# Performance work log

Measured on AMD Instinct MI355X. Metric: run time of the kernel, lower is better.

The kernel has to match this reference:

```python
import jax, jax.numpy as jnp
import numpy as np

N = 100000
E = 1600000
C_IN = 32
HEADS = 4
C = 32          # per-head out channels
L = 3           # num layers = num_hidden_layers + 1
NEG_SLOPE = 0.2


def setup_inputs() -> dict:
    key = jax.random.key(0)
    ks = jax.random.split(key, 8)
    x = jax.random.normal(ks[0], (N, C_IN), dtype=jnp.float32)
    edge_index = jax.random.randint(ks[1], (2, E), 0, N, dtype=jnp.int64)
    edge_attr = jax.random.normal(ks[2], (E, 8), dtype=jnp.float32)  # unused by GATConv (edge_dim=None)
    scale = 1.0 / np.sqrt(C_IN)
    Ws = jax.random.normal(ks[3], (L, C_IN, HEADS * C), dtype=jnp.float32) * scale
    att_src = jax.random.normal(ks[4], (L, HEADS, C), dtype=jnp.float32) * scale
    att_dst = jax.random.normal(ks[5], (L, HEADS, C), dtype=jnp.float32) * scale
    bias = jnp.zeros((L, C), dtype=jnp.float32)
    return {"x": x, "edge_index": edge_index, "edge_attr": edge_attr,
            "Ws": Ws, "att_src": att_src, "att_dst": att_dst, "bias": bias}


def _gat_layer(x, src, dst, W, a_src, a_dst, b):
    # x: [N, C_in]; src/dst: [E'] (self-loops included); W: [C_in, H*C]
    h = (x @ W).reshape(N, HEADS, C)                      # [N, H, C]
    alpha_src = jnp.sum(h * a_src, axis=-1)               # [N, H]
    alpha_dst = jnp.sum(h * a_dst, axis=-1)               # [N, H]
    e = alpha_src[src] + alpha_dst[dst]                   # [E', H]
    e = jnp.where(e > 0, e, NEG_SLOPE * e)                # leaky_relu
    # segment softmax over incoming edges of each dst node
    m = jax.ops.segment_max(e, dst, num_segments=N)       # [N, H]
    ex = jnp.exp(e - m[dst])
    s = jax.ops.segment_sum(ex, dst, num_segments=N)      # [N, H]
    alpha = ex / (s[dst] + 1e-16)                         # [E', H]
    msg = h[src] * alpha[:, :, None]                      # [E', H, C]
    out = jax.ops.segment_sum(msg, dst, num_segments=N)   # [N, H, C]
    return out.mean(axis=1) + b                           # concat=False -> mean over heads, + bias


def reference(x, edge_index, edge_attr, Ws, att_src, att_dst, bias):
    # add self loops once (GATConv add_self_loops=True)
    loops = jnp.arange(N, dtype=edge_index.dtype)
    src = jnp.concatenate([edge_index[0], loops])
    dst = jnp.concatenate([edge_index[1], loops])
    # edge_attr unused: GATConv built without edge_dim.
    # Dropout layers are identity in eval mode.
    for l in range(L):
        x = _gat_layer(x, src, dst, Ws[l], att_src[l], att_dst[l], bias[l])
        x = jax.nn.elu(x)
    return x
```

## Files before the change

kernel.cpp:

```cpp
#include <hip/hip_runtime.h>
#include <hip/hip_bf16.h>
#include <hip/hip_fp16.h>
#include <cstdint>


__global__ void k_scan1(const int* __restrict__ deg, int n, int* __restrict__ bsums) {
    __shared__ int s[256];
    int t = threadIdx.x;
    int i = blockIdx.x * 256 + t;
    int v = (i < n) ? deg[i] : 0;
    s[t] = v; __syncthreads();
    for (int off = 128; off > 0; off >>= 1) {
        if (t < off) s[t] += s[t + off];
        __syncthreads();
    }
    if (t == 0) bsums[blockIdx.x] = s[0];
}

__global__ void k_scan2(const int* __restrict__ bsums, int nb, int* __restrict__ boffs) {
    __shared__ int s[512];
    int t = threadIdx.x;
    int v = (t < nb) ? bsums[t] : 0;
    s[t] = v; __syncthreads();
    for (int off = 1; off < 512; off <<= 1) {
        int nv = (t >= off) ? s[t - off] : 0;
        __syncthreads();
        s[t] += nv;
        __syncthreads();
    }
    if (t < nb) boffs[t] = s[t] - v;
}

__global__ void k_scan3(const int* __restrict__ deg, int n, const int* __restrict__ boffs,
                        int* __restrict__ rowst) {
    __shared__ int s[256];
    int t = threadIdx.x;
    int i = blockIdx.x * 256 + t;
    int v = (i < n) ? deg[i] : 0;
    s[t] = v; __syncthreads();
    for (int off = 1; off < 256; off <<= 1) {
        int nv = (t >= off) ? s[t - off] : 0;
        __syncthreads();
        s[t] += nv;
        __syncthreads();
    }
    int incl = s[t] + boffs[blockIdx.x];
    if (i < n) {
        rowst[i] = incl - v;
        if (i == n - 1) rowst[n] = incl;
    }
}

__global__ void k_scatter(const int* __restrict__ src, const int* __restrict__ dst,
                          const int* __restrict__ rank, const int* __restrict__ rowst,
                          int E, int* __restrict__ col) {
    int t = blockIdx.x * blockDim.x + threadIdx.x;
    int base = t * 16;
    if (base + 16 <= E) {
        int4 d[4], s[4], r[4];
#pragma unroll
        for (int k = 0; k < 4; ++k) {
            d[k] = *reinterpret_cast<const int4*>(dst + base + k * 4);
            s[k] = *reinterpret_cast<const int4*>(src + base + k * 4);
            r[k] = *reinterpret_cast<const int4*>(rank + base + k * 4);
        }
        const int* dd = reinterpret_cast<const int*>(d);
        const int* ss = reinterpret_cast<const int*>(s);
        const int* rr = reinterpret_cast<const int*>(r);
        int p[16];
#pragma unroll
        for (int k = 0; k < 16; ++k) p[k] = rowst[dd[k]] + rr[k];
#pragma unroll
        for (int k = 0; k < 16; ++k) col[p[k]] = ss[k];
    } else {
        for (int i = base; i < E; ++i) col[rowst[dst[i]] + rank[i]] = src[i];
    }
}


__device__ __forceinline__ float lane_bcast(float v, int k) {
    return __int_as_float(__builtin_amdgcn_readlane(__float_as_int(v), k));
}

__global__ void __launch_bounds__(256)
k_gemm_alpha(const float* __restrict__ x, const float* __restrict__ W,
             const float* __restrict__ a_src, const float* __restrict__ a_dst,
             __half* __restrict__ h16, float* __restrict__ alpha_src,
             float* __restrict__ alpha_dst, int n,
             const int* __restrict__ dstv, int E, int* __restrict__ deg,
             int* __restrict__ rank, int gemmBlocks) {
    if ((int)blockIdx.x >= gemmBlocks) {
        int b = blockIdx.x - gemmBlocks;
        int base = (b * 256 + threadIdx.x) * 32;
        if (base + 32 <= E) {
            int4 d[8];
#pragma unroll
            for (int k = 0; k < 8; ++k)
                d[k] = *reinterpret_cast<const int4*>(dstv + base + k * 4);
            const int* dd = reinterpret_cast<const int*>(d);
            int r[32];
#pragma unroll
            for (int k = 0; k < 32; ++k) r[k] = atomicAdd(&deg[dd[k]], 1);
#pragma unroll
            for (int k = 0; k < 8; ++k)
                *reinterpret_cast<int4*>(rank + base + k * 4) =
                    *reinterpret_cast<const int4*>(r + k * 4);
        } else {
            for (int i = base; i < E; ++i) rank[i] = atomicAdd(&deg[dstv[i]], 1);
        }
        return;
    }
    int lane = threadIdx.x & 63;
    int wave = threadIdx.x >> 6;
    int j2 = lane * 2;
    int nbase = blockIdx.x * 64 + wave * 16;

    float2 wr[32];
#pragma unroll
    for (int k = 0; k < 32; ++k)
        wr[k] = *reinterpret_cast<const float2*>(W + k * 128 + j2);
    float2 as2 = *reinterpret_cast<const float2*>(a_src + j2);
    float2 ad2 = *reinterpret_cast<const float2*>(a_dst + j2);

    float xr[16];
#pragma unroll
    for (int m = 0; m < 16; ++m) {
        int node = nbase + m;
        xr[m] = (node < n) ? x[(size_t)node * 32 + (lane & 31)] : 0.f;
    }

#pragma unroll
    for (int m = 0; m < 16; ++m) {
        int node = nbase + m;
        if (node >= n) continue;
        float acc0 = 0.f, acc1 = 0.f;
#pragma unroll
        for (int k = 0; k < 32; ++k) {
            float xv = lane_bcast(xr[m], k);
            acc0 += xv * wr[k].x;
            acc1 += xv * wr[k].y;
        }
        *reinterpret_cast<__half2*>(h16 + (size_t)node * 128 + j2) =
            __floats2half2_rn(acc0, acc1);
        float ps = acc0 * as2.x + acc1 * as2.y;
        float pd = acc0 * ad2.x + acc1 * ad2.y;
#pragma unroll
        for (int mm = 1; mm < 16; mm <<= 1) {
            ps += __shfl_xor(ps, mm, 64);
            pd += __shfl_xor(pd, mm, 64);
        }
        if ((lane & 15) == 0) {
            int head = lane >> 4;
            alpha_src[node * 4 + head] = ps;
            alpha_dst[node * 4 + head] = pd;
        }
    }
}

__device__ __forceinline__ float lrelu_exp(float e) {
    e = e > 0.f ? e : 0.2f * e;
    return __expf(e);
}

__device__ __forceinline__ float4 h16_to_f4(uint2 v) {
    float2 fa = __half22float2(*reinterpret_cast<__half2*>(&v.x));
    float2 fb = __half22float2(*reinterpret_cast<__half2*>(&v.y));
    return make_float4(fa.x, fa.y, fb.x, fb.y);
}

__global__ void k_agg(const __half* __restrict__ h16, const float* __restrict__ asrc,
                      const float* __restrict__ adst, const int* __restrict__ rowst,
                      const int* __restrict__ col, const float* __restrict__ bias,
                      float* __restrict__ out, int n) {
    int wid = (int)((blockIdx.x * (size_t)blockDim.x + threadIdx.x) >> 6);
    if (wid >= n) return;
    int lane = threadIdx.x & 63;
    int half = lane >> 5;
    int q = lane & 31;
    int head = q >> 3;
    float ad = adst[wid * 4 + head];

    float4 acc = make_float4(0.f, 0.f, 0.f, 0.f);
    float s = 0.f;
    if (half == 0) {
        float w = lrelu_exp(asrc[wid * 4 + head] + ad);
        uint2 v = *reinterpret_cast<const uint2*>(h16 + (size_t)wid * 128 + q * 4);
        float4 hv = h16_to_f4(v);
        s = w;
        acc.x = w * hv.x; acc.y = w * hv.y; acc.z = w * hv.z; acc.w = w * hv.w;
    }

    int beg = rowst[wid], end = rowst[wid + 1];
    int i = beg;
    for (; i + 8 <= end; i += 8) {
        int base = i + half * 4;
        int s0 = col[base], s1 = col[base + 1], s2 = col[base + 2], s3 = col[base + 3];
        float x0 = asrc[s0 * 4 + head];
        float x1 = asrc[s1 * 4 + head];
        float x2 = asrc[s2 * 4 + head];
        float x3 = asrc[s3 * 4 + head];
        uint2 v0 = *reinterpret_cast<const uint2*>(h16 + (size_t)s0 * 128 + q * 4);
        uint2 v1 = *reinterpret_cast<const uint2*>(h16 + (size_t)s1 * 128 + q * 4);
        uint2 v2 = *reinterpret_cast<const uint2*>(h16 + (size_t)s2 * 128 + q * 4);
        uint2 v3 = *reinterpret_cast<const uint2*>(h16 + (size_t)s3 * 128 + q * 4);
        float w0 = lrelu_exp(x0 + ad);
        float w1 = lrelu_exp(x1 + ad);
        float w2 = lrelu_exp(x2 + ad);
        float w3 = lrelu_exp(x3 + ad);
        float4 h0 = h16_to_f4(v0), h1 = h16_to_f4(v1), h2 = h16_to_f4(v2), h3 = h16_to_f4(v3);
        s += w0 + w1 + w2 + w3;
        acc.x += w0 * h0.x + w1 * h1.x + w2 * h2.x + w3 * h3.x;
        acc.y += w0 * h0.y + w1 * h1.y + w2 * h2.y + w3 * h3.y;
        acc.z += w0 * h0.z + w1 * h1.z + w2 * h2.z + w3 * h3.z;
        acc.w += w0 * h0.w + w1 * h1.w + w2 * h2.w + w3 * h3.w;
    }
    for (; i + 2 <= end; i += 2) {
        int sidx = col[i + half];
        float w = lrelu_exp(asrc[sidx * 4 + head] + ad);
        float4 hv = h16_to_f4(*reinterpret_cast<const uint2*>(h16 + (size_t)sidx * 128 + q * 4));
        s += w;
        acc.x += w * hv.x; acc.y += w * hv.y; acc.z += w * hv.z; acc.w += w * hv.w;
    }
    if (i < end && half == 0) {
        int sidx = col[i];
        float w = lrelu_exp(asrc[sidx * 4 + head] + ad);
        float4 hv = h16_to_f4(*reinterpret_cast<const uint2*>(h16 + (size_t)sidx * 128 + q * 4));
        s += w;
        acc.x += w * hv.x; acc.y += w * hv.y; acc.z += w * hv.z; acc.w += w * hv.w;
    }

    s += __shfl_xor(s, 32, 64);
    acc.x += __shfl_xor(acc.x, 32, 64);
    acc.y += __shfl_xor(acc.y, 32, 64);
    acc.z += __shfl_xor(acc.z, 32, 64);
    acc.w += __shfl_xor(acc.w, 32, 64);
    float inv = 1.f / s;
    acc.x *= inv; acc.y *= inv; acc.z *= inv; acc.w *= inv;
    acc.x += __shfl_xor(acc.x, 8, 64);  acc.x += __shfl_xor(acc.x, 16, 64);
    acc.y += __shfl_xor(acc.y, 8, 64);  acc.y += __shfl_xor(acc.y, 16, 64);
    acc.z += __shfl_xor(acc.z, 8, 64);  acc.z += __shfl_xor(acc.z, 16, 64);
    acc.w += __shfl_xor(acc.w, 8, 64);  acc.w += __shfl_xor(acc.w, 16, 64);
    if (lane < 8) {
        float4 b4 = *reinterpret_cast<const float4*>(&bias[lane * 4]);
        float o0 = acc.x * 0.25f + b4.x;
        float o1 = acc.y * 0.25f + b4.y;
        float o2 = acc.z * 0.25f + b4.z;
        float o3 = acc.w * 0.25f + b4.w;
        o0 = o0 > 0.f ? o0 : (__expf(o0) - 1.f);
        o1 = o1 > 0.f ? o1 : (__expf(o1) - 1.f);
        o2 = o2 > 0.f ? o2 : (__expf(o2) - 1.f);
        o3 = o3 > 0.f ? o3 : (__expf(o3) - 1.f);
        *reinterpret_cast<float4*>(&out[(size_t)wid * 32 + lane * 4]) =
            make_float4(o0, o1, o2, o3);
    }
}


extern "C" void kernel_launch(void* const* d_in, const int* in_sizes, int n_in,
                              void* d_out, int out_size, void* d_ws, size_t ws_size,
                              hipStream_t stream) {
    const float* x       = (const float*)d_in[0];
    const int*   ei      = (const int*)d_in[1];
    const float* Ws      = (const float*)d_in[3];
    const float* att_src = (const float*)d_in[4];
    const float* att_dst = (const float*)d_in[5];
    const float* bias    = (const float*)d_in[6];

    int N = in_sizes[0] / 32;
    int E = in_sizes[1] / 2;
    const int* srcv = ei;
    const int* dstv = ei + E;

    float* fws   = (float*)d_ws;
    __half* h16  = (__half*)fws;
    float* asrc  = (float*)(h16 + (size_t)N * 128);
    float* adst  = asrc + (size_t)N * 4;
    float* xbuf  = adst + (size_t)N * 4;
    int*   deg    = (int*)(xbuf + (size_t)N * 32);
    int*   rowst  = deg + N;
    int*   bsums  = rowst + N + 1;
    int*   boffs  = bsums + 512;
    int*   col    = boffs + 512;
    int*   rank   = col + E;

    int nb256 = (N + 255) / 256;
    int gemmBlocks = (N + 63) / 64;
    int histBlocks = (E + 32 * 256 - 1) / (32 * 256);
    int scatBlocks = (E + 16 * 256 - 1) / (16 * 256);

    hipMemsetAsync(deg, 0, (size_t)N * sizeof(int), stream);

    for (int l = 0; l < 3; ++l) {
        const float* xin = (l == 0) ? x : xbuf;
        float* xout = (l == 2) ? (float*)d_out : xbuf;
        int extra = (l == 0) ? histBlocks : 0;
        k_gemm_alpha<<<gemmBlocks + extra, 256, 0, stream>>>(
            xin, Ws + (size_t)l * 32 * 128, att_src + l * 128, att_dst + l * 128,
            h16, asrc, adst, N, dstv, E, deg, rank, gemmBlocks);
        if (l == 0) {
            k_scan1<<<nb256, 256, 0, stream>>>(deg, N, bsums);
            k_scan2<<<1, 512, 0, stream>>>(bsums, nb256, boffs);
            k_scan3<<<nb256, 256, 0, stream>>>(deg, N, boffs, rowst);
            k_scatter<<<scatBlocks, 256, 0, stream>>>(srcv, dstv, rank, rowst, E, col);
        }
        k_agg<<<(N + 3) / 4, 256, 0, stream>>>(
            h16, asrc, adst, rowst, col, bias + l * 32, xout, N);
    }
}
```

Before: 437.7 us.

## Split aggregation wavefront into four 16-lane edge groups with 16-byte loads

The aggregation kernel now splits each wavefront into four 16-lane groups. Each lane loads 8 fp16 features (uint4) per neighbor instead of 4, so four edges are gathered concurrently instead of two. This is meant to raise memory-level parallelism and use wider gathers for short adjacency lists. In exchange it needs more accumulator registers and more cross-lane shuffle reductions, and lanes go idle when a node's degree is not a multiple of four.

```diff
diff --git a/kernel.cpp b/kernel.cpp
--- a/kernel.cpp
+++ b/kernel.cpp
@@ -162,12 +162,6 @@
     return __expf(e);
 }
 
-__device__ __forceinline__ float4 h16_to_f4(uint2 v) {
-    float2 fa = __half22float2(*reinterpret_cast<__half2*>(&v.x));
-    float2 fb = __half22float2(*reinterpret_cast<__half2*>(&v.y));
-    return make_float4(fa.x, fa.y, fb.x, fb.y);
-}
-
 __global__ void k_agg(const __half* __restrict__ h16, const float* __restrict__ asrc,
                       const float* __restrict__ adst, const int* __restrict__ rowst,
                       const int* __restrict__ col, const float* __restrict__ bias,
@@ -175,83 +169,88 @@
     int wid = (int)((blockIdx.x * (size_t)blockDim.x + threadIdx.x) >> 6);
     if (wid >= n) return;
     int lane = threadIdx.x & 63;
-    int half = lane >> 5;
-    int q = lane & 31;
-    int head = q >> 3;
+    int g = lane >> 4;
+    int q = lane & 15;
+    int head = q >> 2;
     float ad = adst[wid * 4 + head];
 
-    float4 acc = make_float4(0.f, 0.f, 0.f, 0.f);
+    float acc[8] = {0.f, 0.f, 0.f, 0.f, 0.f, 0.f, 0.f, 0.f};
     float s = 0.f;
-    if (half == 0) {
+
+    if (g == 0) {
         float w = lrelu_exp(asrc[wid * 4 + head] + ad);
-        uint2 v = *reinterpret_cast<const uint2*>(h16 + (size_t)wid * 128 + q * 4);
-        float4 hv = h16_to_f4(v);
+        uint4 v = *reinterpret_cast<const uint4*>(h16 + (size_t)wid * 128 + q * 8);
+        const __half2* hp = reinterpret_cast<const __half2*>(&v);
         s = w;
-        acc.x = w * hv.x; acc.y = w * hv.y; acc.z = w * hv.z; acc.w = w * hv.w;
+#pragma unroll
+        for (int k = 0; k < 4; ++k) {
+            float2 f = __half22float2(hp[k]);
+            acc[2 * k]     += w * f.x;
+            acc[2 * k + 1] += w * f.y;
+        }
     }
 
     int beg = rowst[wid], end = rowst[wid + 1];
-    int i = beg;
-    for (; i + 8 <= end; i += 8) {
-        int base = i + half * 4;
-        int s0 = col[base], s1 = col[base + 1], s2 = col[base + 2], s3 = col[base + 3];
+    int i = beg + g;
+    for (; i + 4 < end; i += 8) {
+        int s0 = col[i];
+        int s1 = col[i + 4];
         float x0 = asrc[s0 * 4 + head];
         float x1 = asrc[s1 * 4 + head];
-        float x2 = asrc[s2 * 4 + head];
-        float x3 = asrc[s3 * 4 + head];
-        uint2 v0 = *reinterpret_cast<const uint2*>(h16 + (size_t)s0 * 128 + q * 4);
-        uint2 v1 = *reinterpret_cast<const uint2*>(h16 + (size_t)s1 * 128 + q * 4);
-        uint2 v2 = *reinterpret_cast<const uint2*>(h16 + (size_t)s2 * 128 + q * 4);
-        uint2 v3 = *reinterpret_cast<const uint2*>(h16 + (size_t)s3 * 128 + q * 4);
+        uint4 v0 = *reinterpret_cast<const uint4*>(h16 + (size_t)s0 * 128 + q * 8);
+        uint4 v1 = *reinterpret_cast<const uint4*>(h16 + (size_t)s1 * 128 + q * 8);
         float w0 = lrelu_exp(x0 + ad);
         float w1 = lrelu_exp(x1 + ad);
-        float w2 = lrelu_exp(x2 + ad);
-        float w3 = lrelu_exp(x3 + ad);
-        float4 h0 = h16_to_f4(v0), h1 = h16_to_f4(v1), h2 = h16_to_f4(v2), h3 = h16_to_f4(v3);
-        s += w0 + w1 + w2 + w3;
-        acc.x += w0 * h0.x + w1 * h1.x + w2 * h2.x + w3 * h3.x;
-        acc.y += w0 * h0.y + w1 * h1.y + w2 * h2.y + w3 * h3.y;
-        acc.z += w0 * h0.z + w1 * h1.z + w2 * h2.z + w3 * h3.z;
-        acc.w += w0 * h0.w + w1 * h1.w + w2 * h2.w + w3 * h3.w;
-    }
-    for (; i + 2 <= end; i += 2) {
-        int sidx = col[i + half];
-        float w = lrelu_exp(asrc[sidx * 4 + head] + ad);
-        float4 hv = h16_to_f4(*reinterpret_cast<const uint2*>(h16 + (size_t)sidx * 128 + q * 4));
+        s += w0 + w1;
+        const __half2* h0 = reinterpret_cast<const __half2*>(&v0);
+        const __half2* h1 = reinterpret_cast<const __half2*>(&v1);
+#pragma unroll
+        for (int k = 0; k < 4; ++k) {
+            float2 f0 = __half22float2(h0[k]);
+            float2 f1 = __half22float2(h1[k]);
+            acc[2 * k]     += w0 * f0.x + w1 * f1.x;
+            acc[2 * k + 1] += w0 * f0.y + w1 * f1.y;
+        }
+    }
+    if (i < end) {
+        int s0 = col[i];
+        float w = lrelu_exp(asrc[s0 * 4 + head] + ad);
+        uint4 v = *reinterpret_cast<const uint4*>(h16 + (size_t)s0 * 128 + q * 8);
+        const __half2* hp = reinterpret_cast<const __half2*>(&v);
         s += w;
-        acc.x += w * hv.x; acc.y += w * hv.y; acc.z += w * hv.z; acc.w += w * hv.w;
-    }
-    if (i < end && half == 0) {
-        int sidx = col[i];
-        float w = lrelu_exp(asrc[sidx * 4 + head] + ad);
-        float4 hv = h16_to_f4(*reinterpret_cast<const uint2*>(h16 + (size_t)sidx * 128 + q * 4));
-        s += w;
-        acc.x += w * hv.x; acc.y += w * hv.y; acc.z += w * hv.z; acc.w += w * hv.w;
-    }
-
+#pragma unroll
+        for (int k = 0; k < 4; ++k) {
+            float2 f = __half22float2(hp[k]);
+            acc[2 * k]     += w * f.x;
+            acc[2 * k + 1] += w * f.y;
+        }
+    }
+
+    s += __shfl_xor(s, 16, 64);
     s += __shfl_xor(s, 32, 64);
-    acc.x += __shfl_xor(acc.x, 32, 64);
-    acc.y += __shfl_xor(acc.y, 32, 64);
-    acc.z += __shfl_xor(acc.z, 32, 64);
-    acc.w += __shfl_xor(acc.w, 32, 64);
+#pragma unroll
+    for (int k = 0; k < 8; ++k) {
+        acc[k] += __shfl_xor(acc[k], 16, 64);
+        acc[k] += __shfl_xor(acc[k], 32, 64);
+    }
     float inv = 1.f / s;
-    acc.x *= inv; acc.y *= inv; acc.z *= inv; acc.w *= inv;
-    acc.x += __shfl_xor(acc.x, 8, 64);  acc.x += __shfl_xor(acc.x, 16, 64);
-    acc.y += __shfl_xor(acc.y, 8, 64);  acc.y += __shfl_xor(acc.y, 16, 64);
-    acc.z += __shfl_xor(acc.z, 8, 64);  acc.z += __shfl_xor(acc.z, 16, 64);
-    acc.w += __shfl_xor(acc.w, 8, 64);  acc.w += __shfl_xor(acc.w, 16, 64);
-    if (lane < 8) {
-        float4 b4 = *reinterpret_cast<const float4*>(&bias[lane * 4]);
-        float o0 = acc.x * 0.25f + b4.x;
-        float o1 = acc.y * 0.25f + b4.y;
-        float o2 = acc.z * 0.25f + b4.z;
-        float o3 = acc.w * 0.25f + b4.w;
-        o0 = o0 > 0.f ? o0 : (__expf(o0) - 1.f);
-        o1 = o1 > 0.f ? o1 : (__expf(o1) - 1.f);
-        o2 = o2 > 0.f ? o2 : (__expf(o2) - 1.f);
-        o3 = o3 > 0.f ? o3 : (__expf(o3) - 1.f);
-        *reinterpret_cast<float4*>(&out[(size_t)wid * 32 + lane * 4]) =
-            make_float4(o0, o1, o2, o3);
+#pragma unroll
+    for (int k = 0; k < 8; ++k) acc[k] *= inv;
+#pragma unroll
+    for (int k = 0; k < 8; ++k) {
+        acc[k] += __shfl_xor(acc[k], 4, 64);
+        acc[k] += __shfl_xor(acc[k], 8, 64);
+    }
+    if (lane < 4) {
+        float o[8];
+#pragma unroll
+        for (int k = 0; k < 8; ++k) {
+            float v = acc[k] * 0.25f + bias[lane * 8 + k];
+            o[k] = v > 0.f ? v : (__expf(v) - 1.f);
+        }
+        float4* op = reinterpret_cast<float4*>(&out[(size_t)wid * 32 + lane * 8]);
+        op[0] = make_float4(o[0], o[1], o[2], o[3]);
+        op[1] = make_float4(o[4], o[5], o[6], o[7]);
     }
 }
 
```

New measurement: 426.5 us. -2.6%, faster.
